# Optimization experiments

Hardware: AMD Instinct MI355X
Metric: run time of the kernel (lower is better)

## Reference

```python
import jax, jax.numpy as jnp
import numpy as np

# Module hyperparameters (from init_kwargs)
N_HEAD = 16
D_K = 64
D_V = 64
TEMPERATURE = 0.7
TOP_K = 32
NEG_MIN = jnp.finfo(jnp.float32).min


def setup_inputs() -> dict:
    key = jax.random.key(0)
    ks = jax.random.split(key, 7)
    B, L, E = 2, 2048, 1024
    return {
        "q": jax.random.normal(ks[0], (B, L, E), jnp.float32),
        "k": jax.random.normal(ks[1], (B, L, E), jnp.float32),
        "v": jax.random.normal(ks[2], (B, L, D_V), jnp.float32),
        "w_q": jax.random.normal(ks[3], (N_HEAD * D_K, E), jnp.float32) * (E ** -0.5),
        "w_k": jax.random.normal(ks[4], (N_HEAD * D_K, E), jnp.float32) * (E ** -0.5),
        "w_v": jax.random.normal(ks[5], (N_HEAD * D_V, D_V), jnp.float32) * (D_V ** -0.5),
        "w_fc": jax.random.normal(ks[6], (D_V, N_HEAD * D_V), jnp.float32) * ((N_HEAD * D_V) ** -0.5),
    }


def _topk_restrict(logits):
    # Keep exactly TOP_K entries per row (scatter of top-k indices), fill rest with dtype min.
    B, H, Lq, Lk = logits.shape
    _, idx = jax.lax.top_k(logits, TOP_K)  # [B,H,Lq,TOP_K]
    bb = jnp.arange(B)[:, None, None, None]
    hh = jnp.arange(H)[None, :, None, None]
    qq = jnp.arange(Lq)[None, None, :, None]
    keep = jnp.zeros(logits.shape, bool).at[bb, hh, qq, idx].set(True)
    return jnp.where(keep, logits, NEG_MIN)


def reference(q, k, v, w_q, w_k, w_v, w_fc):
    B, Lq, _ = q.shape
    Lk = k.shape[1]
    Lv = v.shape[1]
    # Projections (bias-free linears), split heads: [B, H, L, d]
    q_proj = (q @ w_q.T).reshape(B, Lq, N_HEAD, D_K).transpose(0, 2, 1, 3)
    k_proj = (k @ w_k.T).reshape(B, Lk, N_HEAD, D_K).transpose(0, 2, 1, 3)
    v_proj = (v @ w_v.T).reshape(B, Lv, N_HEAD, D_V).transpose(0, 2, 1, 3)
    # Scaled QK^T in float32, then temperature scaling.
    logits = jnp.einsum("bhqd,bhkd->bhqk", q_proj / (D_K ** 0.5), k_proj).astype(jnp.float32)
    logits = logits / TEMPERATURE
    # Top-k restriction of attention logits (query_mask_flat=None -> applied to all queries).
    logits = _topk_restrict(logits)
    # Softmax selection; dropout is identity in eval / p=0.
    attn_probs = jax.nn.softmax(logits, axis=-1).astype(v.dtype)
    mixed = jnp.einsum("bhqk,bhkd->bhqd", attn_probs, v_proj)
    out = mixed.transpose(0, 2, 1, 3).reshape(B, Lq, N_HEAD * D_V)
    output = out @ w_fc.T
    return output, attn_probs
```

## Files before the change

kernel.cpp:

```cpp
#include <hip/hip_runtime.h>
#include <stdint.h>
#include <float.h>

constexpr int L = 2048;
constexpr int H = 16;
constexpr float SCALE = 0.17857142857142858f;
constexpr int OUT0 = 2 * 2048 * 64;
constexpr float QSTEP = 0.0625f;

typedef float f32x4 __attribute__((ext_vector_type(4)));
typedef short s16x8 __attribute__((ext_vector_type(8)));
typedef unsigned short u16x8 __attribute__((ext_vector_type(8)));
typedef _Float16 h16x8 __attribute__((ext_vector_type(8)));

__device__ __forceinline__ float wave_fmax(float x) {
#pragma unroll
  for (int s = 32; s; s >>= 1) x = fmaxf(x, __shfl_xor(x, s));
  return x;
}
__device__ __forceinline__ float wave_fsum(float x) {
#pragma unroll
  for (int s = 32; s; s >>= 1) x += __shfl_xor(x, s);
  return x;
}
__device__ __forceinline__ int wave_isum(int x) {
#pragma unroll
  for (int s = 32; s; s >>= 1) x += __shfl_xor(x, s);
  return x;
}
__device__ __forceinline__ unsigned f2sort(float f) {
  unsigned u = __float_as_uint(f);
  return (u & 0x80000000u) ? ~u : (u | 0x80000000u);
}
__device__ __forceinline__ void lds_fence() {
  __asm__ __volatile__("s_waitcnt lgkmcnt(0)" ::: "memory");
}

__device__ __forceinline__ void gload_lds16(const void* g, void* l) {
  __builtin_amdgcn_global_load_lds((const __attribute__((address_space(1))) void*)g,
                                   (__attribute__((address_space(3))) void*)l, 16, 0, 0);
}

__global__ __launch_bounds__(256) void split_kernel(
    const float* __restrict__ q, const float* __restrict__ k,
    const float* __restrict__ wq, const float* __restrict__ wk,
    unsigned short* __restrict__ qh, unsigned short* __restrict__ ql,
    unsigned short* __restrict__ kh, unsigned short* __restrict__ kl,
    unsigned short* __restrict__ wqh, unsigned short* __restrict__ wql,
    unsigned short* __restrict__ wkh, unsigned short* __restrict__ wkl) {
  const int y = blockIdx.y;
  const float* src = (y == 0) ? q : (y == 1) ? k : (y == 2) ? wq : wk;
  unsigned short* dh = (y == 0) ? qh : (y == 1) ? kh : (y == 2) ? wqh : wkh;
  unsigned short* dl = (y == 0) ? ql : (y == 1) ? kl : (y == 2) ? wql : wkl;
  const int n = (y < 2) ? (4096 * 1024) : (1024 * 1024);
  int idx = (blockIdx.x * 256 + threadIdx.x) * 4;
  const int stride = gridDim.x * 256 * 4;
  for (; idx < n; idx += stride) {
    float4 v = *(const float4*)(src + idx);
    float xs[4] = {v.x, v.y, v.z, v.w};
    unsigned short hs[4], ls[4];
#pragma unroll
    for (int i = 0; i < 4; ++i) {
      float x = xs[i] * 256.0f;
      _Float16 hh = (_Float16)x;
      float r = x - (float)hh;
      _Float16 ll = (_Float16)r;
      hs[i] = __builtin_bit_cast(unsigned short, hh);
      ls[i] = __builtin_bit_cast(unsigned short, ll);
    }
    *(ushort4*)(dh + idx) = make_ushort4(hs[0], hs[1], hs[2], hs[3]);
    *(ushort4*)(dl + idx) = make_ushort4(ls[0], ls[1], ls[2], ls[3]);
  }
}

__global__ __launch_bounds__(256) void proj_split_kernel(
    const unsigned short* __restrict__ QH, const unsigned short* __restrict__ QL,
    const unsigned short* __restrict__ KH, const unsigned short* __restrict__ KL,
    const unsigned short* __restrict__ WQH, const unsigned short* __restrict__ WQL,
    const unsigned short* __restrict__ WKH, const unsigned short* __restrict__ WKL,
    float* __restrict__ QP, float* __restrict__ KP,
    unsigned short* __restrict__ Q16, unsigned short* __restrict__ K16) {
  __shared__ unsigned short sh[4][128 * 64];
  const int t = threadIdx.x;
  const int z = blockIdx.z;
  const int m0 = blockIdx.y * 128;
  const int n0 = blockIdx.x * 128;
  const unsigned short* xh = z ? KH : QH;
  const unsigned short* xl = z ? KL : QL;
  const unsigned short* wh = z ? WKH : WQH;
  const unsigned short* wl = z ? WKL : WQL;
  float* Y = z ? KP : QP;
  unsigned short* Y16 = z ? K16 : Q16;
  const unsigned short* mats[4] = {xh + (size_t)m0 * 1024, xl + (size_t)m0 * 1024,
                                   wh + (size_t)n0 * 1024, wl + (size_t)n0 * 1024};
  const int wv = t >> 6, lane = t & 63;
  const int wm = (wv & 1) * 64, wn = (wv >> 1) * 64;
  const int fr = lane & 15, quad = lane >> 4;
  f32x4 acc[16];
#pragma unroll
  for (int i = 0; i < 16; ++i) acc[i] = (f32x4){0.f, 0.f, 0.f, 0.f};

  for (int c = 0; c < 16; ++c) {
    const int k0 = c * 64;
#pragma unroll
    for (int j = 0; j < 16; ++j) {
      const int mat = j >> 2;
      const int idx = (j & 3) * 256 + t;
      const int r = idx >> 3, p = idx & 7;
      const int sb = p ^ (r & 7);
      gload_lds16(mats[mat] + (size_t)r * 1024 + k0 + sb * 8, &sh[mat][idx * 8]);
    }
    __syncthreads();
#pragma unroll
    for (int kh2 = 0; kh2 < 2; ++kh2) {
      h16x8 ah[4], alv[4], bh[4], blv[4];
#pragma unroll
      for (int mi = 0; mi < 4; ++mi) {
        int row = wm + mi * 16 + fr;
        int pp = (kh2 * 4 + quad) ^ (row & 7);
        ah[mi]  = *(const h16x8*)&sh[0][row * 64 + pp * 8];
        alv[mi] = *(const h16x8*)&sh[1][row * 64 + pp * 8];
      }
#pragma unroll
      for (int ni = 0; ni < 4; ++ni) {
        int row = wn + ni * 16 + fr;
        int pp = (kh2 * 4 + quad) ^ (row & 7);
        bh[ni]  = *(const h16x8*)&sh[2][row * 64 + pp * 8];
        blv[ni] = *(const h16x8*)&sh[3][row * 64 + pp * 8];
      }
#pragma unroll
      for (int mi = 0; mi < 4; ++mi)
#pragma unroll
        for (int ni = 0; ni < 4; ++ni) {
          acc[mi * 4 + ni] = __builtin_amdgcn_mfma_f32_16x16x32_f16(ah[mi], bh[ni], acc[mi * 4 + ni], 0, 0, 0);
          acc[mi * 4 + ni] = __builtin_amdgcn_mfma_f32_16x16x32_f16(ah[mi], blv[ni], acc[mi * 4 + ni], 0, 0, 0);
          acc[mi * 4 + ni] = __builtin_amdgcn_mfma_f32_16x16x32_f16(alv[mi], bh[ni], acc[mi * 4 + ni], 0, 0, 0);
        }
    }
    __syncthreads();
  }
#pragma unroll
  for (int mi = 0; mi < 4; ++mi)
#pragma unroll
    for (int ni = 0; ni < 4; ++ni) {
      int col = n0 + wn + ni * 16 + fr;
      int h = col >> 6, d = col & 63;
#pragma unroll
      for (int r = 0; r < 4; ++r) {
        int m = m0 + wm + mi * 16 + quad * 4 + r;
        int b = m >> 11, l = m & 2047;
        size_t off = (((size_t)b * H + h) * L + l) * 64 + d;
        float val = acc[mi * 4 + ni][r] * (1.0f / 65536.0f);
        Y[off] = val;
        _Float16 hf = (_Float16)val;
        Y16[off] = __builtin_bit_cast(unsigned short, hf);
      }
    }
}

template <int K, bool EMIT>
__global__ __launch_bounds__(256) void proj_kernel(const float* __restrict__ X,
                                                   const float* __restrict__ W,
                                                   float* __restrict__ Y,
                                                   unsigned short* __restrict__ Yb,
                                                   float bscale) {
  __shared__ float As[16][128];
  __shared__ float Bs[16][64];
  const int t = threadIdx.x;
  const int tx = t & 15;
  const int ty = t >> 4;
  const int m0 = blockIdx.y * 128;
  const int n0 = blockIdx.x * 64;
  const int ar = t >> 1, ac = (t & 1) * 8;
  const int br = t >> 2, bc = (t & 3) * 4;
  const float* xg = X + (size_t)(m0 + ar) * K + ac;
  const float* wg = W + (size_t)(n0 + br) * K + bc;
  float acc[8][4] = {};
  for (int k0 = 0; k0 < K; k0 += 16) {
    float4 a0 = *(const float4*)(xg + k0);
    float4 a1 = *(const float4*)(xg + k0 + 4);
    float4 b0 = *(const float4*)(wg + k0);
    __syncthreads();
    As[ac + 0][ar] = a0.x; As[ac + 1][ar] = a0.y; As[ac + 2][ar] = a0.z; As[ac + 3][ar] = a0.w;
    As[ac + 4][ar] = a1.x; As[ac + 5][ar] = a1.y; As[ac + 6][ar] = a1.z; As[ac + 7][ar] = a1.w;
    Bs[bc + 0][br] = b0.x; Bs[bc + 1][br] = b0.y; Bs[bc + 2][br] = b0.z; Bs[bc + 3][br] = b0.w;
    __syncthreads();
#pragma unroll
    for (int kk = 0; kk < 16; ++kk) {
      float4 av0 = *(const float4*)&As[kk][ty * 8];
      float4 av1 = *(const float4*)&As[kk][ty * 8 + 4];
      float4 bv = *(const float4*)&Bs[kk][tx * 4];
      float ar8[8] = {av0.x, av0.y, av0.z, av0.w, av1.x, av1.y, av1.z, av1.w};
      float br4[4] = {bv.x, bv.y, bv.z, bv.w};
#pragma unroll
      for (int i = 0; i < 8; ++i)
#pragma unroll
        for (int j = 0; j < 4; ++j) acc[i][j] = fmaf(ar8[i], br4[j], acc[i][j]);
    }
  }
  const int n = n0 + tx * 4;
  const int h = n >> 6, d = n & 63;
#pragma unroll
  for (int i = 0; i < 8; ++i) {
    int mm = m0 + ty * 8 + i;
    int b = mm >> 11, l = mm & 2047;
    size_t off = (((size_t)b * H + h) * L + l) * 64 + d;
    *(float4*)&Y[off] = make_float4(acc[i][0], acc[i][1], acc[i][2], acc[i][3]);
  }
}

constexpr int ALD = 72;
constexpr int CTB = 136;

__global__ __launch_bounds__(256) void alogits_kernel(const unsigned short* __restrict__ Qb,
                                                      const unsigned short* __restrict__ Kb,
                                                      char* __restrict__ AL) {
  __shared__ union {
    unsigned short qk[2][128 * ALD];
    char ct[128 * CTB];
  } sh;
  const int t = threadIdx.x;
  const int bh = blockIdx.z;
  const int m0 = blockIdx.y * 128, n0 = blockIdx.x * 128;
  const unsigned short* Qg = Qb + (size_t)bh * L * 64 + (size_t)m0 * 64;
  const unsigned short* Kg = Kb + (size_t)bh * L * 64 + (size_t)n0 * 64;
#pragma unroll
  for (int i = 0; i < 4; ++i) {
    int blk = t * 4 + i;
    int r = blk >> 3, lb = blk & 7;
    *(u16x8*)&sh.qk[0][r * ALD + lb * 8] = *(const u16x8*)&Qg[r * 64 + lb * 8];
    *(u16x8*)&sh.qk[1][r * ALD + lb * 8] = *(const u16x8*)&Kg[r * 64 + lb * 8];
  }
  __syncthreads();
  const int wv = t >> 6, lane = t & 63;
  const int wm = (wv & 1) * 64, wn = (wv >> 1) * 64;
  const int fr = lane & 15, quad = lane >> 4;
  f32x4 acc[16];
#pragma unroll
  for (int i = 0; i < 16; ++i) acc[i] = (f32x4){0.f, 0.f, 0.f, 0.f};
#pragma unroll
  for (int kh = 0; kh < 2; ++kh) {
    h16x8 a[4], b[4];
#pragma unroll
    for (int mi = 0; mi < 4; ++mi)
      a[mi] = *(const h16x8*)&sh.qk[0][(wm + mi * 16 + fr) * ALD + kh * 32 + quad * 8];
#pragma unroll
    for (int ni = 0; ni < 4; ++ni)
      b[ni] = *(const h16x8*)&sh.qk[1][(wn + ni * 16 + fr) * ALD + kh * 32 + quad * 8];
#pragma unroll
    for (int mi = 0; mi < 4; ++mi)
#pragma unroll
      for (int ni = 0; ni < 4; ++ni)
        acc[mi * 4 + ni] = __builtin_amdgcn_mfma_f32_16x16x32_f16(
            a[mi], b[ni], acc[mi * 4 + ni], 0, 0, 0);
  }
  __syncthreads();
#pragma unroll
  for (int mi = 0; mi < 4; ++mi)
#pragma unroll
    for (int ni = 0; ni < 4; ++ni) {
      int col = wn + ni * 16 + fr;
#pragma unroll
      for (int r = 0; r < 4; ++r) {
        int rowl = wm + mi * 16 + quad * 4 + r;
        float sc = acc[mi * 4 + ni][r] * 2.8571428571428572f;
        sc = fminf(fmaxf(sc, -127.0f), 127.0f);
        sh.ct[rowl * CTB + col] = (char)__float2int_rn(sc);
      }
    }
  __syncthreads();
  char* Abase = AL + (size_t)bh * L * L;
  const int rq = lane >> 4;
  const int cq = (lane & 15) * 8;
#pragma unroll
  for (int it = 0; it < 8; ++it) {
    int row = wv * 32 + it * 4 + rq;
    uint2 v8 = *(const uint2*)&sh.ct[row * CTB + cq];
    __builtin_nontemporal_store(v8.x, (unsigned*)&Abase[(size_t)(m0 + row) * L + n0 + cq]);
    __builtin_nontemporal_store(v8.y, (unsigned*)&Abase[(size_t)(m0 + row) * L + n0 + cq + 4]);
  }
}

__global__ __launch_bounds__(256) void select_kernel(const char* __restrict__ AL,
                                                     const float* __restrict__ Qp,
                                                     const float* __restrict__ Kp,
                                                     const float* __restrict__ Vp,
                                                     float* __restrict__ Probs,
                                                     float* __restrict__ Mixed) {
  __shared__ float prow[4][2048];
  __shared__ float qbuf[4][64];
  __shared__ float cbuf[4][64];
  __shared__ int ibufc[4][64];
  __shared__ float pbuf[4][32];
  __shared__ int ibuf[4][32];
  const int lane = threadIdx.x & 63;
  const int w = threadIdx.x >> 6;
  const int row = blockIdx.x * 4 + w;
  const int bh = row >> 11;
  const int q = row & 2047;
  const unsigned long long below = (lane == 63) ? 0x7fffffffffffffffull
                                                : ((1ull << lane) - 1ull);
  const unsigned* Arow = (const unsigned*)(AL + (size_t)row * 2048);

  float lg[32];
#pragma unroll
  for (int u2 = 0; u2 < 8; ++u2) {
    unsigned dw = __builtin_nontemporal_load(Arow + u2 * 64 + lane);
#pragma unroll
    for (int b = 0; b < 4; ++b)
      lg[u2 * 4 + b] = (float)((char)(dw >> (8 * b))) * QSTEP;
  }
#pragma unroll
  for (int u = 0; u < 32; ++u) prow[w][u * 64 + lane] = 0.f;
  if (lane < 16)
    *(float4*)&qbuf[w][lane * 4] = *(const float4*)&Qp[((size_t)bh * L + q) * 64 + lane * 4];

  float m = lg[0];
#pragma unroll
  for (int u = 1; u < 32; ++u) m = fmaxf(m, lg[u]);
  m = wave_fmax(m);

  float T = 0.f;
  bool found = false;
  float cut = m - 2.2f;
  float lo = 0.f, hi = m;
  bool has_lo = false;
  for (int attempt = 0; attempt < 8 && !found; ++attempt) {
    int c = 0;
#pragma unroll
    for (int u = 0; u < 32; ++u) c += (lg[u] > cut) ? 1 : 0;
    c = wave_isum(c);
    if (c < 32) {
      hi = cut;
      cut = has_lo ? 0.5f * (lo + cut) : (cut - 0.45f);
    } else if (c > 64) {
      lo = cut; has_lo = true;
      cut = 0.5f * (cut + hi);
    } else {
      int base = 0;
#pragma unroll
      for (int u = 0; u < 32; ++u) {
        bool cd = lg[u] > cut;
        unsigned long long mk = __ballot(cd);
        if (cd) cbuf[w][base + __popcll(mk & below)] = lg[u];
        base += __popcll(mk);
      }
      lds_fence();
      float v2 = (lane < c) ? cbuf[w][lane] : -FLT_MAX;
#pragma unroll
      for (int size = 2; size <= 64; size <<= 1)
#pragma unroll
        for (int stride = size >> 1; stride; stride >>= 1) {
          float pv = __shfl_xor(v2, stride);
          bool lower = (lane & stride) == 0;
          bool asc = (lane & size) == 0;
          v2 = (lower == asc) ? fminf(v2, pv) : fmaxf(v2, pv);
        }
      T = __shfl(v2, 32);
      found = true;
    }
  }
  if (!found) {
    unsigned tb = 0;
    for (int bit = 31; bit >= 0; --bit) {
      unsigned cand = tb | (1u << bit);
      int c = 0;
#pragma unroll
      for (int u = 0; u < 32; ++u) c += (f2sort(lg[u]) >= cand) ? 1 : 0;
      c = wave_isum(c);
      if (c >= 32) tb = cand;
    }
    T = (tb & 0x80000000u) ? __uint_as_float(tb & 0x7fffffffu) : __uint_as_float(~tb);
  }

  float theta = T;
  int c2 = 0;
  const float margs[5] = {0.40f, 0.25f, 0.15f, 0.08f, 0.0f};
#pragma unroll
  for (int a = 0; a < 5; ++a) {
    float th = T - margs[a];
    int c = 0;
#pragma unroll
    for (int u = 0; u < 32; ++u) c += (lg[u] >= th) ? 1 : 0;
    c = wave_isum(c);
    theta = th; c2 = c;
    if (c <= 64) break;
  }
  if (c2 > 64) c2 = 64;

  {
    int base = 0;
#pragma unroll
    for (int u = 0; u < 32; ++u) {
      bool cd = lg[u] >= theta;
      unsigned long long mk = __ballot(cd);
      if (cd) {
        int s = base + __popcll(mk & below);
        if (s < 64) ibufc[w][s] = ((u >> 2) * 64 + lane) * 4 + (u & 3);
      }
      base += __popcll(mk);
    }
  }
  lds_fence();

  int myi = (lane < c2) ? ibufc[w][lane] : 0x7fffffff;
  float vex = -FLT_MAX;
  if (lane < c2) {
    const float4* K4 = (const float4*)(Kp + ((size_t)bh * L + myi) * 64);
    const float4* Q4 = (const float4*)&qbuf[w][0];
    float acc = 0.f;
#pragma unroll
    for (int dq = 0; dq < 16; ++dq) {
      float4 kv = K4[dq];
      float4 qv = Q4[dq];
      acc = fmaf(qv.x, kv.x, acc);
      acc = fmaf(qv.y, kv.y, acc);
      acc = fmaf(qv.z, kv.z, acc);
      acc = fmaf(qv.w, kv.w, acc);
    }
    vex = (acc * 0.125f) / 0.7f;
  }

  unsigned long long key = ((unsigned long long)(~f2sort(vex)) << 32) | (unsigned)myi;
#pragma unroll
  for (int size = 2; size <= 64; size <<= 1)
#pragma unroll
    for (int stride = size >> 1; stride; stride >>= 1) {
      unsigned long long pk = __shfl_xor(key, stride);
      unsigned long long mn = key < pk ? key : pk;
      unsigned long long mx = key < pk ? pk : key;
      bool keepmin = ((lane & stride) == 0) == ((lane & size) == 0);
      key = keepmin ? mn : mx;
    }
  unsigned uv = ~(unsigned)(key >> 32);
  float vs = __uint_as_float((uv & 0x80000000u) ? (uv & 0x7fffffffu) : ~uv);
  int sidx = (int)(unsigned)(key & 0xffffffffull);

  float vmax = __shfl(vs, 0);
  float e = (lane < 32) ? __expf(vs - vmax) : 0.f;
  float S = wave_fsum(e);
  float p = e / S;
  if (lane < 32) {
    pbuf[w][lane] = p;
    ibuf[w][lane] = sidx;
    prow[w][sidx] = p;
  }
  lds_fence();

  float* Prow = Probs + (size_t)row * 2048;
#pragma unroll
  for (int u = 0; u < 32; ++u)
    __builtin_nontemporal_store(prow[w][u * 64 + lane], Prow + u * 64 + lane);

  const float* Vb = Vp + (size_t)bh * L * 64;
  float accv = 0.f;
#pragma unroll
  for (int i = 0; i < 32; ++i)
    accv = fmaf(pbuf[w][i], Vb[(size_t)ibuf[w][i] * 64 + lane], accv);
  const int bb = bh >> 4, hh = bh & 15;
  Mixed[((size_t)(bb * 2048 + q)) * 1024 + hh * 64 + lane] = accv;
}

__global__ __launch_bounds__(256) void fc_kernel(const float* __restrict__ Mx,
                                                 const float* __restrict__ Wfc,
                                                 float* __restrict__ Out) {
  __shared__ float As[32][64];
  __shared__ float Ws[64][64];
  const int t = threadIdx.x;
  const int tx = t & 15;
  const int ty = t >> 4;
  const int m0 = blockIdx.x * 32;
  float acc[2][4] = {};
  for (int k0 = 0; k0 < 1024; k0 += 64) {
    __syncthreads();
    {
      int lin = t * 8;
      int rr = lin >> 6, kk = lin & 63;
      *(float4*)&As[rr][kk] = *(const float4*)&Mx[(size_t)(m0 + rr) * 1024 + k0 + kk];
      *(float4*)&As[rr][kk + 4] = *(const float4*)&Mx[(size_t)(m0 + rr) * 1024 + k0 + kk + 4];
    }
    {
      int n = t >> 2;
      int kq = (t & 3) * 16;
#pragma unroll
      for (int u = 0; u < 4; ++u) {
        float4 wv = *(const float4*)&Wfc[(size_t)n * 1024 + k0 + kq + u * 4];
        Ws[kq + u * 4 + 0][n] = wv.x;
        Ws[kq + u * 4 + 1][n] = wv.y;
        Ws[kq + u * 4 + 2][n] = wv.z;
        Ws[kq + u * 4 + 3][n] = wv.w;
      }
    }
    __syncthreads();
#pragma unroll
    for (int kk = 0; kk < 64; ++kk) {
      float a0 = As[ty][kk], a1 = As[ty + 16][kk];
      float4 wv = *(const float4*)&Ws[kk][tx * 4];
      float wr[4] = {wv.x, wv.y, wv.z, wv.w};
#pragma unroll
      for (int j = 0; j < 4; ++j) {
        acc[0][j] = fmaf(a0, wr[j], acc[0][j]);
        acc[1][j] = fmaf(a1, wr[j], acc[1][j]);
      }
    }
  }
#pragma unroll
  for (int i = 0; i < 2; ++i) {
    int mm = m0 + ty + i * 16;
    *(float4*)&Out[(size_t)mm * 64 + tx * 4] =
        make_float4(acc[i][0], acc[i][1], acc[i][2], acc[i][3]);
  }
}

extern "C" void kernel_launch(void* const* d_in, const int* in_sizes, int n_in,
                              void* d_out, int out_size, void* d_ws, size_t ws_size,
                              hipStream_t stream) {
  const float* q    = (const float*)d_in[0];
  const float* k    = (const float*)d_in[1];
  const float* v    = (const float*)d_in[2];
  const float* w_q  = (const float*)d_in[3];
  const float* w_k  = (const float*)d_in[4];
  const float* w_v  = (const float*)d_in[5];
  const float* w_fc = (const float*)d_in[6];

  float* out = (float*)d_out;
  float* probs = out + OUT0;

  float* ws = (float*)d_ws;
  float* q_proj = ws;
  float* k_proj = ws + 4194304;
  float* v_proj = ws + 8388608;
  float* mixed  = ws + 12582912;
  unsigned short* qb = (unsigned short*)(ws + 16777216);
  unsigned short* kb = (unsigned short*)(ws + 18874368);
  char* al = (char*)(ws + 20971520);

  unsigned short* qh  = (unsigned short*)((char*)d_ws + 234881024);
  unsigned short* ql  = qh + 4194304;
  unsigned short* kh  = ql + 4194304;
  unsigned short* kl  = kh + 4194304;
  unsigned short* wqh = kl + 4194304;
  unsigned short* wql = wqh + 1048576;
  unsigned short* wkh = wql + 1048576;
  unsigned short* wkl = wkh + 1048576;

  dim3 blk(256);
  split_kernel<<<dim3(1024, 4), blk, 0, stream>>>(q, k, w_q, w_k,
                                                  qh, ql, kh, kl, wqh, wql, wkh, wkl);
  proj_split_kernel<<<dim3(8, 32, 2), blk, 0, stream>>>(qh, ql, kh, kl,
                                                        wqh, wql, wkh, wkl,
                                                        q_proj, k_proj, qb, kb);
  proj_kernel<64, false><<<dim3(16, 32), blk, 0, stream>>>(v, w_v, v_proj, nullptr, 1.0f);
  alogits_kernel<<<dim3(16, 16, 32), blk, 0, stream>>>(qb, kb, al);
  select_kernel<<<dim3(16384), blk, 0, stream>>>(al, q_proj, k_proj, v_proj, probs, mixed);
  fc_kernel<<<dim3(128), blk, 0, stream>>>(mixed, w_fc, out);
}
```

Before: 875.9 us.

## Overlap next-chunk global-to-LDS loads with MFMA in projection GEMM

```diff
diff --git a/kernel.cpp b/kernel.cpp
--- a/kernel.cpp
+++ b/kernel.cpp
@@ -73,7 +73,7 @@
   }
 }
 
-__global__ __launch_bounds__(256) void proj_split_kernel(
+__global__ __launch_bounds__(256, 2) void proj_split_kernel(
     const unsigned short* __restrict__ QH, const unsigned short* __restrict__ QL,
     const unsigned short* __restrict__ KH, const unsigned short* __restrict__ KL,
     const unsigned short* __restrict__ WQH, const unsigned short* __restrict__ WQL,
@@ -100,45 +100,53 @@
 #pragma unroll
   for (int i = 0; i < 16; ++i) acc[i] = (f32x4){0.f, 0.f, 0.f, 0.f};
 
+#define STAGE(cc)                                                              \
+  {                                                                            \
+    const int k0s = (cc) * 64;                                                 \
+    _Pragma("unroll") for (int j = 0; j < 16; ++j) {                           \
+      const int mat = j >> 2;                                                  \
+      const int idx = (j & 3) * 256 + t;                                       \
+      const int r = idx >> 3, p = idx & 7;                                     \
+      const int sb = p ^ (r & 7);                                              \
+      gload_lds16(mats[mat] + (size_t)r * 1024 + k0s + sb * 8, &sh[mat][idx * 8]); \
+    }                                                                          \
+  }
+
+  STAGE(0);
   for (int c = 0; c < 16; ++c) {
-    const int k0 = c * 64;
-#pragma unroll
-    for (int j = 0; j < 16; ++j) {
-      const int mat = j >> 2;
-      const int idx = (j & 3) * 256 + t;
-      const int r = idx >> 3, p = idx & 7;
-      const int sb = p ^ (r & 7);
-      gload_lds16(mats[mat] + (size_t)r * 1024 + k0 + sb * 8, &sh[mat][idx * 8]);
-    }
     __syncthreads();
+    h16x8 ah[2][4], alv[2][4], bh[2][4], blv[2][4];
 #pragma unroll
     for (int kh2 = 0; kh2 < 2; ++kh2) {
-      h16x8 ah[4], alv[4], bh[4], blv[4];
 #pragma unroll
       for (int mi = 0; mi < 4; ++mi) {
         int row = wm + mi * 16 + fr;
         int pp = (kh2 * 4 + quad) ^ (row & 7);
-        ah[mi]  = *(const h16x8*)&sh[0][row * 64 + pp * 8];
-        alv[mi] = *(const h16x8*)&sh[1][row * 64 + pp * 8];
+        ah[kh2][mi]  = *(const h16x8*)&sh[0][row * 64 + pp * 8];
+        alv[kh2][mi] = *(const h16x8*)&sh[1][row * 64 + pp * 8];
       }
 #pragma unroll
       for (int ni = 0; ni < 4; ++ni) {
         int row = wn + ni * 16 + fr;
         int pp = (kh2 * 4 + quad) ^ (row & 7);
-        bh[ni]  = *(const h16x8*)&sh[2][row * 64 + pp * 8];
-        blv[ni] = *(const h16x8*)&sh[3][row * 64 + pp * 8];
-      }
+        bh[kh2][ni]  = *(const h16x8*)&sh[2][row * 64 + pp * 8];
+        blv[kh2][ni] = *(const h16x8*)&sh[3][row * 64 + pp * 8];
+      }
+    }
+    __syncthreads();
+    if (c < 15) STAGE(c + 1);
+#pragma unroll
+    for (int kh2 = 0; kh2 < 2; ++kh2)
 #pragma unroll
       for (int mi = 0; mi < 4; ++mi)
 #pragma unroll
         for (int ni = 0; ni < 4; ++ni) {
-          acc[mi * 4 + ni] = __builtin_amdgcn_mfma_f32_16x16x32_f16(ah[mi], bh[ni], acc[mi * 4 + ni], 0, 0, 0);
-          acc[mi * 4 + ni] = __builtin_amdgcn_mfma_f32_16x16x32_f16(ah[mi], blv[ni], acc[mi * 4 + ni], 0, 0, 0);
-          acc[mi * 4 + ni] = __builtin_amdgcn_mfma_f32_16x16x32_f16(alv[mi], bh[ni], acc[mi * 4 + ni], 0, 0, 0);
+          acc[mi * 4 + ni] = __builtin_amdgcn_mfma_f32_16x16x32_f16(ah[kh2][mi], bh[kh2][ni], acc[mi * 4 + ni], 0, 0, 0);
+          acc[mi * 4 + ni] = __builtin_amdgcn_mfma_f32_16x16x32_f16(ah[kh2][mi], blv[kh2][ni], acc[mi * 4 + ni], 0, 0, 0);
+          acc[mi * 4 + ni] = __builtin_amdgcn_mfma_f32_16x16x32_f16(alv[kh2][mi], bh[kh2][ni], acc[mi * 4 + ni], 0, 0, 0);
         }
-    }
-    __syncthreads();
-  }
+  }
+#undef STAGE
 #pragma unroll
   for (int mi = 0; mi < 4; ++mi)
 #pragma unroll
```

After: 862.7 us. No clear change (-1.5%).
